# Kernel optimization log

Hardware: AMD Instinct MI355X
Metric: run time of the kernel (lower is better)

## Reference

```python
import jax, jax.numpy as jnp
import numpy as np

TOP_K = 2

def setup_inputs() -> dict:
    key = jax.random.key(0)
    k1, k2 = jax.random.split(key)
    B, S, D, E = 4, 8192, 1024, 64
    hidden_states = jax.random.normal(k1, (B, S, D), dtype=jnp.float32)
    gate_weight = jax.random.normal(k2, (E, D), dtype=jnp.float32) * (1.0 / D ** 0.5)
    return {"hidden_states": hidden_states, "gate_weight": gate_weight}

def reference(hidden_states, gate_weight):
    # router_logits: [B, S, E] = hidden @ W^T
    router_logits = jnp.einsum('bsd,ed->bse', hidden_states, gate_weight)
    # softmax in float32 (matches .float() in torch), cast back to input dtype
    router_probs = jax.nn.softmax(router_logits.astype(jnp.float32), axis=-1).astype(hidden_states.dtype)
    top_k_probs, selected_experts = jax.lax.top_k(router_probs, TOP_K)
    top_k_probs = top_k_probs / (jnp.sum(top_k_probs, axis=-1, keepdims=True) + 1e-08)
    return top_k_probs, selected_experts, router_logits
```

## Files before the change

### kernel.cpp

```cpp
#include <hip/hip_runtime.h>
#include <math.h>


typedef __attribute__((ext_vector_type(8))) short bf16x8;
typedef __attribute__((ext_vector_type(4))) float f32x4;

static constexpr int TOKENS = 32768;
static constexpr int DDIM   = 1024;
static constexpr int NEXP   = 64;
static constexpr size_t OFF_EXP = 65536;
static constexpr size_t OFF_LOG = 131072;

__global__ void w_split3_kernel(const float* __restrict__ w,
                                short* __restrict__ w1,
                                short* __restrict__ w2,
                                short* __restrict__ w3) {
    int idx = blockIdx.x * blockDim.x + threadIdx.x;
    for (int i = idx; i < NEXP * DDIM; i += gridDim.x * blockDim.x) {
        int e = i >> 10, k = i & 1023;
        float f = w[i];
        unsigned u1 = __float_as_uint(f);
        float f1 = __uint_as_float(u1 & 0xffff0000u);
        float r1 = f - f1;
        unsigned u2 = __float_as_uint(r1);
        float f2 = __uint_as_float(u2 & 0xffff0000u);
        float r2 = r1 - f2;
        unsigned u3 = __float_as_uint(r2);
        int n = e >> 4, c = k >> 5;
        int lane = (e & 15) + ((k & 31) >> 3) * 16;
        int j = k & 7;
        size_t dst = ((size_t)(c * 4 + n) * 64 + lane) * 8 + j;
        w1[dst] = (short)(u1 >> 16);
        w2[dst] = (short)(u2 >> 16);
        w3[dst] = (short)(u3 >> 16);
    }
}

__device__ inline void split8(float4 a, float4 b,
                              bf16x8& o1, bf16x8& o2, bf16x8& o3) {
    float f[8] = {a.x, a.y, a.z, a.w, b.x, b.y, b.z, b.w};
#pragma unroll
    for (int j = 0; j < 8; ++j) {
        unsigned u1 = __float_as_uint(f[j]);
        float f1 = __uint_as_float(u1 & 0xffff0000u);
        float r1 = f[j] - f1;
        unsigned u2 = __float_as_uint(r1);
        float f2 = __uint_as_float(u2 & 0xffff0000u);
        float r2 = r1 - f2;
        o1[j] = (short)(u1 >> 16);
        o2[j] = (short)(u2 >> 16);
        o3[j] = (short)(__float_as_uint(r2) >> 16);
    }
}

typedef const __attribute__((address_space(1))) unsigned int* gas1_t;
typedef __attribute__((address_space(3))) unsigned int* las3_t;
__device__ inline void stage16(const void* g, void* l) {
    __builtin_amdgcn_global_load_lds((gas1_t)(uintptr_t)g,
                                     (las3_t)(uintptr_t)l, 16, 0, 0);
}

__global__ __launch_bounds__(512, 4)
void router_mfma_kernel(const float* __restrict__ h,
                        const short* __restrict__ w1,
                        const short* __restrict__ w2,
                        const short* __restrict__ w3,
                        float* __restrict__ out) {
    __shared__ alignas(16) char smem[49152];
    const int tid   = threadIdx.x;
    const int lane  = tid & 63;
    const int wv    = tid >> 6;
    const int khalf = wv & 1;
    const int mg    = wv >> 1;
    const int token0 = blockIdx.x * 64 + mg * 16;
    const int arow  = lane & 15;
    const int ks    = lane >> 4;

    const float* ap = h + (size_t)(token0 + arow) * DDIM + khalf * 512 + ks * 8;

    const short* warr[3] = {w1, w2, w3};
    const char* gsrc[3];
    int ldso[3];
#pragma unroll
    for (int i = 0; i < 3; ++i) {
        int seg = wv * 3 + i;
        int kh = seg & 1;
        int an = seg >> 1;
        int a = an >> 2, n = an & 3;
        gsrc[i] = (const char*)warr[a] + (size_t)(kh * 64 + n) * 1024 + lane * 16;
        ldso[i] = (kh * 12 + a * 4 + n) * 1024;
    }

#define STAGE(bb, cc)                                                      \
    {                                                                      \
        _Pragma("unroll")                                                  \
        for (int i = 0; i < 3; ++i)                                        \
            stage16(gsrc[i] + (size_t)(cc) * 4096,                         \
                    smem + (bb) * 24576 + ldso[i]);                        \
    }

    f32x4 acc[4];
#pragma unroll
    for (int n = 0; n < 4; ++n)
#pragma unroll
        for (int r = 0; r < 4; ++r) acc[n][r] = 0.0f;

    float4 ring[3][2];

    STAGE(0, 0);
    ring[0][0] = *reinterpret_cast<const float4*>(ap);
    ring[0][1] = *reinterpret_cast<const float4*>(ap + 4);
    ring[1][0] = *reinterpret_cast<const float4*>(ap + 32);
    ring[1][1] = *reinterpret_cast<const float4*>(ap + 36);
    asm volatile("s_waitcnt vmcnt(4)" ::: "memory");
    __builtin_amdgcn_s_barrier();

#pragma unroll
    for (int t = 0; t < 16; ++t) {
        const int b = t & 1;
        if (t < 15) STAGE(b ^ 1, t + 1);
        if (t < 14) {
            ring[(t + 2) % 3][0] =
                *reinterpret_cast<const float4*>(ap + (t + 2) * 32);
            ring[(t + 2) % 3][1] =
                *reinterpret_cast<const float4*>(ap + (t + 2) * 32 + 4);
        }

        bf16x8 A1f, A2f, A3f;
        split8(ring[t % 3][0], ring[t % 3][1], A1f, A2f, A3f);

        const char* wb = smem + b * 24576 + khalf * 12288 + lane * 16;
#pragma unroll
        for (int n = 0; n < 4; ++n) {
            bf16x8 W1v = *reinterpret_cast<const bf16x8*>(wb + n * 1024);
            bf16x8 W2v = *reinterpret_cast<const bf16x8*>(wb + n * 1024 + 4096);
            bf16x8 W3v = *reinterpret_cast<const bf16x8*>(wb + n * 1024 + 8192);
            f32x4 t2 = acc[n];
            t2 = __builtin_amdgcn_mfma_f32_16x16x32_bf16(A3f, W1v, t2, 0, 0, 0);
            t2 = __builtin_amdgcn_mfma_f32_16x16x32_bf16(A1f, W3v, t2, 0, 0, 0);
            t2 = __builtin_amdgcn_mfma_f32_16x16x32_bf16(A2f, W2v, t2, 0, 0, 0);
            t2 = __builtin_amdgcn_mfma_f32_16x16x32_bf16(A2f, W1v, t2, 0, 0, 0);
            t2 = __builtin_amdgcn_mfma_f32_16x16x32_bf16(A1f, W2v, t2, 0, 0, 0);
            t2 = __builtin_amdgcn_mfma_f32_16x16x32_bf16(A1f, W1v, t2, 0, 0, 0);
            acc[n] = t2;
        }

        if (t < 14) {
            asm volatile("s_waitcnt vmcnt(2)" ::: "memory");
            __builtin_amdgcn_s_barrier();
        } else if (t == 14) {
            asm volatile("s_waitcnt vmcnt(0)" ::: "memory");
            __builtin_amdgcn_s_barrier();
        }
    }

    if (khalf == 1) {
        float* c = (float*)smem + (size_t)(mg * 64 + lane) * 17;
#pragma unroll
        for (int n = 0; n < 4; ++n)
#pragma unroll
            for (int r = 0; r < 4; ++r) c[n * 4 + r] = acc[n][r];
    }
    __syncthreads();
    if (khalf != 0) return;

    {
        const float* c = (const float*)smem + (size_t)(mg * 64 + lane) * 17;
#pragma unroll
        for (int n = 0; n < 4; ++n)
#pragma unroll
            for (int r = 0; r < 4; ++r) acc[n][r] += c[n * 4 + r];
    }

    const int rbase = (lane >> 4) * 4;
    const int col   = lane & 15;

#pragma unroll
    for (int n = 0; n < 4; ++n)
#pragma unroll
        for (int r = 0; r < 4; ++r)
            out[OFF_LOG + (size_t)(token0 + rbase + r) * NEXP + n * 16 + col]
                = acc[n][r];

#pragma unroll
    for (int r = 0; r < 4; ++r) {
        const int token = token0 + rbase + r;
        float mx = fmaxf(fmaxf(acc[0][r], acc[1][r]),
                         fmaxf(acc[2][r], acc[3][r]));
#pragma unroll
        for (int d = 1; d <= 8; d <<= 1) mx = fmaxf(mx, __shfl_xor(mx, d, 64));

        float p[4];
        float s = 0.0f;
#pragma unroll
        for (int n = 0; n < 4; ++n) { p[n] = expf(acc[n][r] - mx); s += p[n]; }
#pragma unroll
        for (int d = 1; d <= 8; d <<= 1) s += __shfl_xor(s, d, 64);

        float v1 = -INFINITY, v2 = -INFINITY;
        int   i1 = NEXP,      i2 = NEXP;
#pragma unroll
        for (int n = 0; n < 4; ++n) {
            float v = p[n];
            int   ei = n * 16 + col;
            if (v > v1)      { v2 = v1; i2 = i1; v1 = v; i1 = ei; }
            else if (v > v2) { v2 = v;  i2 = ei; }
        }

#pragma unroll
        for (int d = 1; d <= 8; d <<= 1) {
            float ov1 = __shfl_xor(v1, d, 64);
            float ov2 = __shfl_xor(v2, d, 64);
            int   oi1 = __shfl_xor(i1, d, 64);
            int   oi2 = __shfl_xor(i2, d, 64);
            bool ofirst = (ov1 > v1) || (ov1 == v1 && oi1 < i1);
            float n1, n2; int ni1, ni2;
            if (ofirst) {
                n1 = ov1; ni1 = oi1;
                bool sec = (v1 > ov2) || (v1 == ov2 && i1 < oi2);
                n2 = sec ? v1 : ov2; ni2 = sec ? i1 : oi2;
            } else {
                n1 = v1; ni1 = i1;
                bool sec = (ov1 > v2) || (ov1 == v2 && oi1 < i2);
                n2 = sec ? ov1 : v2; ni2 = sec ? oi1 : i2;
            }
            v1 = n1; i1 = ni1; v2 = n2; i2 = ni2;
        }

        if (col == 0) {
            float t1 = v1 / s;
            float t2 = v2 / s;
            float dn = t1 + t2 + 1e-8f;
            float2 pr; pr.x = t1 / dn; pr.y = t2 / dn;
            *reinterpret_cast<float2*>(out + (size_t)token * 2) = pr;
            float2 ex; ex.x = (float)i1; ex.y = (float)i2;
            *reinterpret_cast<float2*>(out + OFF_EXP + (size_t)token * 2) = ex;
        }
    }
#undef STAGE
}

extern "C" void kernel_launch(void* const* d_in, const int* in_sizes, int n_in,
                              void* d_out, int out_size, void* d_ws, size_t ws_size,
                              hipStream_t stream) {
    const float* h = (const float*)d_in[0];
    const float* w = (const float*)d_in[1];
    float* out = (float*)d_out;
    short* w1 = (short*)d_ws;
    short* w2 = w1 + (size_t)NEXP * DDIM;
    short* w3 = w2 + (size_t)NEXP * DDIM;
    hipLaunchKernelGGL(w_split3_kernel, dim3(128), dim3(256), 0, stream, w, w1, w2, w3);
    hipLaunchKernelGGL(router_mfma_kernel, dim3(TOKENS / 64), dim3(512), 0, stream,
                       h, w1, w2, w3, out);
}
```

Before: 44.50 us.

## Double tokens per block and triple-buffer weight staging in router GEMM

Each wave now handles two 16-token M tiles (128 tokens per block), so every weight fragment read from LDS feeds twice as many MFMAs and total weight staging traffic is halved. Weight staging moves from a double buffer to a three-slot ring in a larger 72 KB LDS allocation, prefetching two K-steps ahead, while activation loads drop to a two-slot register ring. The added LDS and register use lowers occupancy (launch bounds go from 4 to 2 blocks per CU), and halving the grid to 256 blocks may leave some CUs idle.

```diff
diff --git a/kernel.cpp b/kernel.cpp
--- a/kernel.cpp
+++ b/kernel.cpp
@@ -60,23 +60,24 @@
                                      (las3_t)(uintptr_t)l, 16, 0, 0);
 }
 
-__global__ __launch_bounds__(512, 4)
+__global__ __launch_bounds__(512, 2)
 void router_mfma_kernel(const float* __restrict__ h,
                         const short* __restrict__ w1,
                         const short* __restrict__ w2,
                         const short* __restrict__ w3,
                         float* __restrict__ out) {
-    __shared__ alignas(16) char smem[49152];
+    __shared__ alignas(16) char smem[73728];
     const int tid   = threadIdx.x;
     const int lane  = tid & 63;
     const int wv    = tid >> 6;
     const int khalf = wv & 1;
     const int mg    = wv >> 1;
-    const int token0 = blockIdx.x * 64 + mg * 16;
+    const int token0 = blockIdx.x * 128 + mg * 32;
     const int arow  = lane & 15;
     const int ks    = lane >> 4;
 
-    const float* ap = h + (size_t)(token0 + arow) * DDIM + khalf * 512 + ks * 8;
+    const float* ap0 = h + (size_t)(token0 + arow) * DDIM + khalf * 512 + ks * 8;
+    const float* ap1 = ap0 + (size_t)16 * DDIM;
 
     const short* warr[3] = {w1, w2, w3};
     const char* gsrc[3];
@@ -99,101 +100,129 @@
                     smem + (bb) * 24576 + ldso[i]);                        \
     }
 
-    f32x4 acc[4];
-#pragma unroll
-    for (int n = 0; n < 4; ++n)
-#pragma unroll
-        for (int r = 0; r < 4; ++r) acc[n][r] = 0.0f;
-
-    float4 ring[3][2];
-
+    f32x4 acc[2][4];
+#pragma unroll
+    for (int m = 0; m < 2; ++m)
+#pragma unroll
+        for (int n = 0; n < 4; ++n)
+#pragma unroll
+            for (int r = 0; r < 4; ++r) acc[m][n][r] = 0.0f;
+
+    float4 ringA[2][2][2];
+
+    ringA[0][0][0] = *reinterpret_cast<const float4*>(ap0);
+    ringA[0][0][1] = *reinterpret_cast<const float4*>(ap0 + 4);
+    ringA[0][1][0] = *reinterpret_cast<const float4*>(ap1);
+    ringA[0][1][1] = *reinterpret_cast<const float4*>(ap1 + 4);
     STAGE(0, 0);
-    ring[0][0] = *reinterpret_cast<const float4*>(ap);
-    ring[0][1] = *reinterpret_cast<const float4*>(ap + 4);
-    ring[1][0] = *reinterpret_cast<const float4*>(ap + 32);
-    ring[1][1] = *reinterpret_cast<const float4*>(ap + 36);
-    asm volatile("s_waitcnt vmcnt(4)" ::: "memory");
+    STAGE(1, 1);
+    asm volatile("s_waitcnt vmcnt(3)" ::: "memory");
     __builtin_amdgcn_s_barrier();
 
 #pragma unroll
     for (int t = 0; t < 16; ++t) {
-        const int b = t & 1;
-        if (t < 15) STAGE(b ^ 1, t + 1);
-        if (t < 14) {
-            ring[(t + 2) % 3][0] =
-                *reinterpret_cast<const float4*>(ap + (t + 2) * 32);
-            ring[(t + 2) % 3][1] =
-                *reinterpret_cast<const float4*>(ap + (t + 2) * 32 + 4);
-        }
-
-        bf16x8 A1f, A2f, A3f;
-        split8(ring[t % 3][0], ring[t % 3][1], A1f, A2f, A3f);
-
-        const char* wb = smem + b * 24576 + khalf * 12288 + lane * 16;
+        const int slot  = t & 1;
+        const int nslot = slot ^ 1;
+        if (t + 1 < 16) {
+            ringA[nslot][0][0] =
+                *reinterpret_cast<const float4*>(ap0 + (t + 1) * 32);
+            ringA[nslot][0][1] =
+                *reinterpret_cast<const float4*>(ap0 + (t + 1) * 32 + 4);
+            ringA[nslot][1][0] =
+                *reinterpret_cast<const float4*>(ap1 + (t + 1) * 32);
+            ringA[nslot][1][1] =
+                *reinterpret_cast<const float4*>(ap1 + (t + 1) * 32 + 4);
+        }
+        if (t + 2 < 16) STAGE((t + 2) % 3, t + 2);
+
+        bf16x8 A1a, A2a, A3a, A1b, A2b, A3b;
+        split8(ringA[slot][0][0], ringA[slot][0][1], A1a, A2a, A3a);
+        split8(ringA[slot][1][0], ringA[slot][1][1], A1b, A2b, A3b);
+
+        const char* wb = smem + (t % 3) * 24576 + khalf * 12288 + lane * 16;
 #pragma unroll
         for (int n = 0; n < 4; ++n) {
             bf16x8 W1v = *reinterpret_cast<const bf16x8*>(wb + n * 1024);
             bf16x8 W2v = *reinterpret_cast<const bf16x8*>(wb + n * 1024 + 4096);
             bf16x8 W3v = *reinterpret_cast<const bf16x8*>(wb + n * 1024 + 8192);
-            f32x4 t2 = acc[n];
-            t2 = __builtin_amdgcn_mfma_f32_16x16x32_bf16(A3f, W1v, t2, 0, 0, 0);
-            t2 = __builtin_amdgcn_mfma_f32_16x16x32_bf16(A1f, W3v, t2, 0, 0, 0);
-            t2 = __builtin_amdgcn_mfma_f32_16x16x32_bf16(A2f, W2v, t2, 0, 0, 0);
-            t2 = __builtin_amdgcn_mfma_f32_16x16x32_bf16(A2f, W1v, t2, 0, 0, 0);
-            t2 = __builtin_amdgcn_mfma_f32_16x16x32_bf16(A1f, W2v, t2, 0, 0, 0);
-            t2 = __builtin_amdgcn_mfma_f32_16x16x32_bf16(A1f, W1v, t2, 0, 0, 0);
-            acc[n] = t2;
-        }
-
-        if (t < 14) {
-            asm volatile("s_waitcnt vmcnt(2)" ::: "memory");
+            f32x4 t0 = acc[0][n];
+            t0 = __builtin_amdgcn_mfma_f32_16x16x32_bf16(A3a, W1v, t0, 0, 0, 0);
+            t0 = __builtin_amdgcn_mfma_f32_16x16x32_bf16(A1a, W3v, t0, 0, 0, 0);
+            t0 = __builtin_amdgcn_mfma_f32_16x16x32_bf16(A2a, W2v, t0, 0, 0, 0);
+            t0 = __builtin_amdgcn_mfma_f32_16x16x32_bf16(A2a, W1v, t0, 0, 0, 0);
+            t0 = __builtin_amdgcn_mfma_f32_16x16x32_bf16(A1a, W2v, t0, 0, 0, 0);
+            t0 = __builtin_amdgcn_mfma_f32_16x16x32_bf16(A1a, W1v, t0, 0, 0, 0);
+            acc[0][n] = t0;
+            f32x4 t1 = acc[1][n];
+            t1 = __builtin_amdgcn_mfma_f32_16x16x32_bf16(A3b, W1v, t1, 0, 0, 0);
+            t1 = __builtin_amdgcn_mfma_f32_16x16x32_bf16(A1b, W3v, t1, 0, 0, 0);
+            t1 = __builtin_amdgcn_mfma_f32_16x16x32_bf16(A2b, W2v, t1, 0, 0, 0);
+            t1 = __builtin_amdgcn_mfma_f32_16x16x32_bf16(A2b, W1v, t1, 0, 0, 0);
+            t1 = __builtin_amdgcn_mfma_f32_16x16x32_bf16(A1b, W2v, t1, 0, 0, 0);
+            t1 = __builtin_amdgcn_mfma_f32_16x16x32_bf16(A1b, W1v, t1, 0, 0, 0);
+            acc[1][n] = t1;
+        }
+
+        if (t <= 13) {
+            asm volatile("s_waitcnt vmcnt(7)" ::: "memory");
             __builtin_amdgcn_s_barrier();
         } else if (t == 14) {
-            asm volatile("s_waitcnt vmcnt(0)" ::: "memory");
+            asm volatile("s_waitcnt vmcnt(4)" ::: "memory");
             __builtin_amdgcn_s_barrier();
         }
     }
 
     if (khalf == 1) {
-        float* c = (float*)smem + (size_t)(mg * 64 + lane) * 17;
-#pragma unroll
-        for (int n = 0; n < 4; ++n)
-#pragma unroll
-            for (int r = 0; r < 4; ++r) c[n * 4 + r] = acc[n][r];
+        float* cb = (float*)(smem + 24576) + (size_t)(mg * 64 + lane) * 33;
+#pragma unroll
+        for (int m = 0; m < 2; ++m)
+#pragma unroll
+            for (int n = 0; n < 4; ++n)
+#pragma unroll
+                for (int r = 0; r < 4; ++r)
+                    cb[m * 16 + n * 4 + r] = acc[m][n][r];
     }
     __syncthreads();
     if (khalf != 0) return;
 
     {
-        const float* c = (const float*)smem + (size_t)(mg * 64 + lane) * 17;
-#pragma unroll
-        for (int n = 0; n < 4; ++n)
-#pragma unroll
-            for (int r = 0; r < 4; ++r) acc[n][r] += c[n * 4 + r];
+        const float* cb = (const float*)(smem + 24576)
+                        + (size_t)(mg * 64 + lane) * 33;
+#pragma unroll
+        for (int m = 0; m < 2; ++m)
+#pragma unroll
+            for (int n = 0; n < 4; ++n)
+#pragma unroll
+                for (int r = 0; r < 4; ++r)
+                    acc[m][n][r] += cb[m * 16 + n * 4 + r];
     }
 
     const int rbase = (lane >> 4) * 4;
     const int col   = lane & 15;
 
 #pragma unroll
-    for (int n = 0; n < 4; ++n)
-#pragma unroll
-        for (int r = 0; r < 4; ++r)
-            out[OFF_LOG + (size_t)(token0 + rbase + r) * NEXP + n * 16 + col]
-                = acc[n][r];
-
+    for (int m = 0; m < 2; ++m)
+#pragma unroll
+        for (int n = 0; n < 4; ++n)
+#pragma unroll
+            for (int r = 0; r < 4; ++r)
+                out[OFF_LOG + (size_t)(token0 + m * 16 + rbase + r) * NEXP
+                    + n * 16 + col] = acc[m][n][r];
+
+#pragma unroll
+    for (int m = 0; m < 2; ++m)
 #pragma unroll
     for (int r = 0; r < 4; ++r) {
-        const int token = token0 + rbase + r;
-        float mx = fmaxf(fmaxf(acc[0][r], acc[1][r]),
-                         fmaxf(acc[2][r], acc[3][r]));
+        const int token = token0 + m * 16 + rbase + r;
+        float mx = fmaxf(fmaxf(acc[m][0][r], acc[m][1][r]),
+                         fmaxf(acc[m][2][r], acc[m][3][r]));
 #pragma unroll
         for (int d = 1; d <= 8; d <<= 1) mx = fmaxf(mx, __shfl_xor(mx, d, 64));
 
         float p[4];
         float s = 0.0f;
 #pragma unroll
-        for (int n = 0; n < 4; ++n) { p[n] = expf(acc[n][r] - mx); s += p[n]; }
+        for (int n = 0; n < 4; ++n) { p[n] = expf(acc[m][n][r] - mx); s += p[n]; }
 #pragma unroll
         for (int d = 1; d <= 8; d <<= 1) s += __shfl_xor(s, d, 64);
 
@@ -250,6 +279,6 @@
     short* w2 = w1 + (size_t)NEXP * DDIM;
     short* w3 = w2 + (size_t)NEXP * DDIM;
     hipLaunchKernelGGL(w_split3_kernel, dim3(128), dim3(256), 0, stream, w, w1, w2, w3);
-    hipLaunchKernelGGL(router_mfma_kernel, dim3(TOKENS / 64), dim3(512), 0, stream,
+    hipLaunchKernelGGL(router_mfma_kernel, dim3(TOKENS / 128), dim3(512), 0, stream,
                        h, w1, w2, w3, out);
 }
```

Result: slower. 52.07 us (+17.0%).
